# Performance work log

Hardware: AMD Instinct MI355X
Metric: run time of the kernel (lower is better)

The kernel has to match this reference:

```python
import jax, jax.numpy as jnp
import numpy as np

N_NODES = 50000
N_EDGES = 800000
D_IN = 128
D_H = 128
D_OUT = 2
N_GRAPHS = 512
EPS = 1e-5


def _sage(x, src, dst, Wl, bl, Wr):
    # mean aggregation of source features at destination nodes
    msum = jax.ops.segment_sum(x[src], dst, num_segments=N_NODES)
    deg = jax.ops.segment_sum(jnp.ones((src.shape[0],), x.dtype), dst, num_segments=N_NODES)
    agg = msum / jnp.clip(deg, 1.0)[:, None]
    return agg @ Wl.T + bl + x @ Wr.T


def _bn(x, g, b, m, v):
    return (x - m) * jax.lax.rsqrt(v + EPS) * g + b


def setup_inputs() -> dict:
    key = jax.random.key(0)
    ks = jax.random.split(key, 24)
    s = lambda k, shape, fan: (jax.random.normal(k, shape, jnp.float32) / np.sqrt(fan))
    x = jax.random.normal(ks[0], (N_NODES, D_IN), jnp.float32)
    edge_index = jax.random.randint(ks[1], (2, N_EDGES), 0, N_NODES, jnp.int64)
    batch = jnp.sort(jax.random.randint(ks[2], (N_NODES,), 0, N_GRAPHS, jnp.int64))
    inp = {"x": x, "edge_index": edge_index, "batch": batch}
    # SAGEConv layers: lin_l (with bias) on aggregated, lin_r (no bias) on root
    dims = [(D_IN, D_H), (D_H, D_H), (D_H, D_OUT)]
    for i, (di, do) in enumerate(dims):
        inp[f"Wl{i}"] = s(ks[3 + 3 * i], (do, di), di)
        inp[f"bl{i}"] = jnp.zeros((do,), jnp.float32)
        inp[f"Wr{i}"] = s(ks[4 + 3 * i], (do, di), di)
    # BatchNorm (eval mode: running stats)
    for i in range(2):
        inp[f"g{i}"] = jnp.ones((D_H,), jnp.float32)
        inp[f"b{i}"] = jnp.zeros((D_H,), jnp.float32)
        inp[f"m{i}"] = 0.1 * jax.random.normal(ks[12 + 2 * i], (D_H,), jnp.float32)
        inp[f"v{i}"] = jax.random.uniform(ks[13 + 2 * i], (D_H,), jnp.float32, 0.5, 1.5)
    # graph prediction MLP: Linear(2*D_OUT, D_H) -> ReLU -> Linear(D_H, D_OUT)
    inp["mW1"] = s(ks[20], (D_H, 2 * D_OUT), 2 * D_OUT)
    inp["mb1"] = jnp.zeros((D_H,), jnp.float32)
    inp["mW2"] = s(ks[21], (D_OUT, D_H), D_H)
    inp["mb2"] = jnp.zeros((D_OUT,), jnp.float32)
    return inp


def reference(x, edge_index, batch, Wl0, bl0, Wr0, Wl1, bl1, Wr1, Wl2, bl2, Wr2,
              g0, b0, m0, v0, g1, b1, m1, v1, mW1, mb1, mW2, mb2):
    src, dst = edge_index[0], edge_index[1]
    h = _sage(x, src, dst, Wl0, bl0, Wr0)
    h = jax.nn.relu(_bn(h, g0, b0, m0, v0))  # dropout inactive in eval
    h = _sage(h, src, dst, Wl1, bl1, Wr1)
    h = jax.nn.relu(_bn(h, g1, b1, m1, v1))
    h = _sage(h, src, dst, Wl2, bl2, Wr2)  # [N, D_OUT]
    # global mean + max pooling per graph
    cnt = jax.ops.segment_sum(jnp.ones((h.shape[0],), h.dtype), batch, num_segments=N_GRAPHS)
    pmean = jax.ops.segment_sum(h, batch, num_segments=N_GRAPHS) / jnp.clip(cnt, 1.0)[:, None]
    pmax = jax.ops.segment_max(h, batch, num_segments=N_GRAPHS)
    g = jnp.concatenate([pmean, pmax], axis=1)  # [G, 2*D_OUT]
    g = jax.nn.relu(g @ mW1.T + mb1)
    return g @ mW2.T + mb2  # [G, D_OUT]
```

## Files before the change

### kernel.cpp

```cpp
#include <hip/hip_runtime.h>
#include <hip/hip_bf16.h>
#include <float.h>

#define N_NODES 50000
#define N_EDGES 800000
#define D_H 128
#define N_GRAPHS 512
#define EPSV 1e-5f
#define NB_SCAN ((N_NODES + 255) / 256)

__device__ __forceinline__ void atomicMaxF(float* addr, float val) {
    if (val >= 0.0f) atomicMax((int*)addr, __float_as_int(val));
    else atomicMin((unsigned int*)addr, (unsigned int)__float_as_int(val));
}

__global__ void hist_kernel(const int* __restrict__ dst, int* __restrict__ cnt) {
    int e = blockIdx.x * blockDim.x + threadIdx.x;
    if (e < N_EDGES) atomicAdd(&cnt[dst[e]], 1);
}

__global__ __launch_bounds__(256) void scan_local_kernel(const int* __restrict__ cnt,
                                                         int* __restrict__ row_ptr,
                                                         int* __restrict__ bsum) {
    __shared__ int sh[256];
    int t = threadIdx.x;
    int i = blockIdx.x * 256 + t;
    int v = (i < N_NODES) ? cnt[i] : 0;
    sh[t] = v;
    __syncthreads();
    int x = v;
    for (int off = 1; off < 256; off <<= 1) {
        int y = (t >= off) ? sh[t - off] : 0;
        __syncthreads();
        x += y;
        sh[t] = x;
        __syncthreads();
    }
    if (i < N_NODES) row_ptr[i] = x - v;
    if (t == 255) bsum[blockIdx.x] = x;
}

__global__ __launch_bounds__(256) void scan_bsum_kernel(const int* __restrict__ bsum,
                                                        int* __restrict__ bofs) {
    __shared__ int sh[256];
    int t = threadIdx.x;
    int v = (t < NB_SCAN) ? bsum[t] : 0;
    sh[t] = v;
    __syncthreads();
    int x = v;
    for (int off = 1; off < 256; off <<= 1) {
        int y = (t >= off) ? sh[t - off] : 0;
        __syncthreads();
        x += y;
        sh[t] = x;
        __syncthreads();
    }
    if (t < NB_SCAN) bofs[t] = x - v;
}

__global__ __launch_bounds__(256) void scan_add_kernel(int* __restrict__ row_ptr,
                                                       int* __restrict__ wofs,
                                                       const int* __restrict__ bofs,
                                                       float* __restrict__ psum,
                                                       float* __restrict__ pcnt,
                                                       float* __restrict__ pmax) {
    int t = threadIdx.x;
    int i = blockIdx.x * 256 + t;
    if (i < N_NODES) {
        int r = row_ptr[i] + bofs[blockIdx.x];
        row_ptr[i] = r;
        wofs[i] = r;
    }
    if (i == 0) row_ptr[N_NODES] = N_EDGES;
    if (i < N_GRAPHS * 2) { psum[i] = 0.f; pmax[i] = -FLT_MAX; }
    if (i < N_GRAPHS) pcnt[i] = 0.f;
}

__global__ void scatter_kernel(const int* __restrict__ src, const int* __restrict__ dst,
                               int* __restrict__ wofs, int* __restrict__ csr_src) {
    int e = blockIdx.x * blockDim.x + threadIdx.x;
    if (e < N_EDGES) {
        int pos = atomicAdd(&wofs[dst[e]], 1);
        csr_src[pos] = src[e];
    }
}

#define ROWS 32
#define RPW 8
template <int MODE>
__global__ __launch_bounds__(256, 6) void fused_sage_kernel(
    const float* __restrict__ xin,
    const int* __restrict__ row_ptr, const int* __restrict__ csr_src,
    const float* __restrict__ Wl, const float* __restrict__ bl,
    const float* __restrict__ Wr,
    const float* __restrict__ gg, const float* __restrict__ bb,
    const float* __restrict__ mm, const float* __restrict__ vv,
    float* __restrict__ hout,
    const float* __restrict__ Wl2, const float* __restrict__ Wr2,
    float* __restrict__ p2r2) {
    __shared__ float s_agg[ROWS][D_H];
    __shared__ float s_x[ROWS][D_H];
    int row0 = blockIdx.x * ROWS;
    int t = threadIdx.x;
    int lane = t & 63;
    int w = t >> 6;

    const float2* xp = (const float2*)xin;

    for (int rr = 0; rr < RPW; rr++) {
        int r = w * RPW + rr;
        int row = row0 + r;
        float2 vx = make_float2(0.f, 0.f);
        float ax = 0.f, ay = 0.f;
        if (row < N_NODES) {
            vx = xp[(size_t)row * 64 + lane];
            int s0 = row_ptr[row], s1 = row_ptr[row + 1];
            int e = s0;
            for (; e + 7 < s1; e += 8) {
                int i0 = csr_src[e],     i1 = csr_src[e + 1];
                int i2 = csr_src[e + 2], i3 = csr_src[e + 3];
                int i4 = csr_src[e + 4], i5 = csr_src[e + 5];
                int i6 = csr_src[e + 6], i7 = csr_src[e + 7];
                float2 v0 = xp[(size_t)i0 * 64 + lane];
                float2 v1 = xp[(size_t)i1 * 64 + lane];
                float2 v2 = xp[(size_t)i2 * 64 + lane];
                float2 v3 = xp[(size_t)i3 * 64 + lane];
                float2 v4 = xp[(size_t)i4 * 64 + lane];
                float2 v5 = xp[(size_t)i5 * 64 + lane];
                float2 v6 = xp[(size_t)i6 * 64 + lane];
                float2 v7 = xp[(size_t)i7 * 64 + lane];
                ax += ((v0.x + v1.x) + (v2.x + v3.x)) + ((v4.x + v5.x) + (v6.x + v7.x));
                ay += ((v0.y + v1.y) + (v2.y + v3.y)) + ((v4.y + v5.y) + (v6.y + v7.y));
            }
            for (; e + 1 < s1; e += 2) {
                int i0 = csr_src[e], i1 = csr_src[e + 1];
                float2 v0 = xp[(size_t)i0 * 64 + lane];
                float2 v1 = xp[(size_t)i1 * 64 + lane];
                ax += v0.x + v1.x;
                ay += v0.y + v1.y;
            }
            if (e < s1) {
                float2 v0 = xp[(size_t)csr_src[e] * 64 + lane];
                ax += v0.x;
                ay += v0.y;
            }
            float inv = 1.0f / (float)max(s1 - s0, 1);
            ax *= inv;
            ay *= inv;
        }
        ((float2*)s_x[r])[lane] = vx;
        ((float2*)s_agg[r])[lane] = make_float2(ax, ay);
    }

    int j = lane;
    const float4* wl0 = (const float4*)(Wl + (size_t)j * D_H);
    const float4* wl1 = (const float4*)(Wl + (size_t)(j + 64) * D_H);
    const float4* wr0 = (const float4*)(Wr + (size_t)j * D_H);
    const float4* wr1 = (const float4*)(Wr + (size_t)(j + 64) * D_H);

    float acc0[RPW], acc1[RPW];
#pragma unroll
    for (int r = 0; r < RPW; r++) { acc0[r] = 0.f; acc1[r] = 0.f; }

    for (int k0 = 0; k0 < D_H / 4; k0 += 2) {
        float4 a0[2], a1[2], b0[2], b1[2];
#pragma unroll
        for (int q = 0; q < 2; q++) {
            a0[q] = wl0[k0 + q];
            a1[q] = wl1[k0 + q];
            b0[q] = wr0[k0 + q];
            b1[q] = wr1[k0 + q];
        }
#pragma unroll
        for (int r = 0; r < RPW; r++) {
            int row = w * RPW + r;
#pragma unroll
            for (int q = 0; q < 2; q++) {
                float4 xa = ((const float4*)s_agg[row])[k0 + q];
                float4 xx = ((const float4*)s_x[row])[k0 + q];
                acc0[r] += xa.x * a0[q].x + xa.y * a0[q].y + xa.z * a0[q].z + xa.w * a0[q].w
                         + xx.x * b0[q].x + xx.y * b0[q].y + xx.z * b0[q].z + xx.w * b0[q].w;
                acc1[r] += xa.x * a1[q].x + xa.y * a1[q].y + xa.z * a1[q].z + xa.w * a1[q].w
                         + xx.x * b1[q].x + xx.y * b1[q].y + xx.z * b1[q].z + xx.w * b1[q].w;
            }
        }
    }

    float sc0 = gg[j] * rsqrtf(vv[j] + EPSV);
    float sh0 = bb[j] + (bl[j] - mm[j]) * sc0;
    float sc1 = gg[j + 64] * rsqrtf(vv[j + 64] + EPSV);
    float sh1 = bb[j + 64] + (bl[j + 64] - mm[j + 64]) * sc1;

    if (MODE == 0) {
#pragma unroll
        for (int r = 0; r < RPW; r++) {
            int row = row0 + w * RPW + r;
            if (row < N_NODES) {
                hout[(size_t)row * D_H + j] = fmaxf(acc0[r] * sc0 + sh0, 0.f);
                hout[(size_t)row * D_H + j + 64] = fmaxf(acc1[r] * sc1 + sh1, 0.f);
            }
        }
    } else {
        float wl2_0a = Wl2[j],       wl2_0b = Wl2[j + 64];
        float wl2_1a = Wl2[128 + j], wl2_1b = Wl2[192 + j];
        float wr2_0a = Wr2[j],       wr2_0b = Wr2[j + 64];
        float wr2_1a = Wr2[128 + j], wr2_1b = Wr2[192 + j];
#pragma unroll
        for (int r = 0; r < RPW; r++) {
            float v0 = fmaxf(acc0[r] * sc0 + sh0, 0.f);
            float v1 = fmaxf(acc1[r] * sc1 + sh1, 0.f);
            float p0 = v0 * wl2_0a + v1 * wl2_0b;
            float p1 = v0 * wl2_1a + v1 * wl2_1b;
            float p2 = v0 * wr2_0a + v1 * wr2_0b;
            float p3 = v0 * wr2_1a + v1 * wr2_1b;
            for (int off = 32; off; off >>= 1) {
                p0 += __shfl_down(p0, off);
                p1 += __shfl_down(p1, off);
                p2 += __shfl_down(p2, off);
                p3 += __shfl_down(p3, off);
            }
            int row = row0 + w * RPW + r;
            if (lane == 0 && row < N_NODES)
                ((float4*)p2r2)[row] = make_float4(p0, p1, p2, p3);
        }
    }
}

__global__ __launch_bounds__(256) void aggpool_kernel(
    const float* __restrict__ p2r2, const int* __restrict__ row_ptr,
    const int* __restrict__ csr_src, const int* __restrict__ batch,
    const float* __restrict__ bl2,
    float* __restrict__ psum, float* __restrict__ pcnt, float* __restrict__ pmax) {
    int i = blockIdx.x * blockDim.x + threadIdx.x;
    if (i >= N_NODES) return;
    int s0 = row_ptr[i], s1 = row_ptr[i + 1];
    float a0 = 0.f, a1 = 0.f;
    int e = s0;
    for (; e + 3 < s1; e += 4) {
        float2 v0 = ((const float2*)p2r2)[(size_t)csr_src[e] * 2];
        float2 v1 = ((const float2*)p2r2)[(size_t)csr_src[e + 1] * 2];
        float2 v2 = ((const float2*)p2r2)[(size_t)csr_src[e + 2] * 2];
        float2 v3 = ((const float2*)p2r2)[(size_t)csr_src[e + 3] * 2];
        a0 += (v0.x + v1.x) + (v2.x + v3.x);
        a1 += (v0.y + v1.y) + (v2.y + v3.y);
    }
    for (; e < s1; e++) {
        float2 v = ((const float2*)p2r2)[(size_t)csr_src[e] * 2];
        a0 += v.x;
        a1 += v.y;
    }
    float inv = 1.0f / (float)max(s1 - s0, 1);
    float2 r = ((const float2*)p2r2)[(size_t)i * 2 + 1];
    float h0 = a0 * inv + bl2[0] + r.x;
    float h1 = a1 * inv + bl2[1] + r.y;
    int b = batch[i];
    atomicAdd(&psum[b * 2], h0);
    atomicAdd(&psum[b * 2 + 1], h1);
    atomicAdd(&pcnt[b], 1.0f);
    atomicMaxF(&pmax[b * 2], h0);
    atomicMaxF(&pmax[b * 2 + 1], h1);
}

__global__ __launch_bounds__(128) void mlp_kernel(
    const float* __restrict__ psum, const float* __restrict__ pcnt,
    const float* __restrict__ pmax,
    const float* __restrict__ mW1, const float* __restrict__ mb1,
    const float* __restrict__ mW2, const float* __restrict__ mb2,
    float* __restrict__ out) {
    int b = blockIdx.x;
    int t = threadIdx.x;
    float cntv = fmaxf(pcnt[b], 1.0f);
    float g0 = psum[b * 2] / cntv;
    float g1 = psum[b * 2 + 1] / cntv;
    float g2 = pmax[b * 2];
    float g3 = pmax[b * 2 + 1];
    float4 w = ((const float4*)mW1)[t];
    float h = fmaxf(g0 * w.x + g1 * w.y + g2 * w.z + g3 * w.w + mb1[t], 0.f);
    float o0 = h * mW2[t];
    float o1 = h * mW2[128 + t];
    for (int off = 32; off; off >>= 1) {
        o0 += __shfl_down(o0, off);
        o1 += __shfl_down(o1, off);
    }
    __shared__ float sh[4];
    if ((t & 63) == 0) {
        sh[(t >> 6) * 2] = o0;
        sh[(t >> 6) * 2 + 1] = o1;
    }
    __syncthreads();
    if (t == 0) {
        out[b * 2] = sh[0] + sh[2] + mb2[0];
        out[b * 2 + 1] = sh[1] + sh[3] + mb2[1];
    }
}

extern "C" void kernel_launch(void* const* d_in, const int* in_sizes, int n_in,
                              void* d_out, int out_size, void* d_ws, size_t ws_size,
                              hipStream_t stream) {
    const float* x = (const float*)d_in[0];
    const int* ei = (const int*)d_in[1];
    const int* batch = (const int*)d_in[2];
    const float* Wl0 = (const float*)d_in[3];
    const float* bl0 = (const float*)d_in[4];
    const float* Wr0 = (const float*)d_in[5];
    const float* Wl1 = (const float*)d_in[6];
    const float* bl1 = (const float*)d_in[7];
    const float* Wr1 = (const float*)d_in[8];
    const float* Wl2 = (const float*)d_in[9];
    const float* bl2 = (const float*)d_in[10];
    const float* Wr2 = (const float*)d_in[11];
    const float* g0 = (const float*)d_in[12];
    const float* b0 = (const float*)d_in[13];
    const float* m0 = (const float*)d_in[14];
    const float* v0 = (const float*)d_in[15];
    const float* g1 = (const float*)d_in[16];
    const float* b1 = (const float*)d_in[17];
    const float* m1 = (const float*)d_in[18];
    const float* v1 = (const float*)d_in[19];
    const float* mW1 = (const float*)d_in[20];
    const float* mb1 = (const float*)d_in[21];
    const float* mW2 = (const float*)d_in[22];
    const float* mb2 = (const float*)d_in[23];

    const int* src = ei;
    const int* dst = ei + N_EDGES;

    char* ws = (char*)d_ws;
    size_t off = 0;
    auto alloc = [&](size_t bytes) -> char* {
        char* p = ws + off;
        off += (bytes + 255) & ~(size_t)255;
        return p;
    };
    int* cnt = (int*)alloc((size_t)N_NODES * 4);
    int* row_ptr = (int*)alloc((size_t)(N_NODES + 1) * 4);
    int* wofs = (int*)alloc((size_t)N_NODES * 4);
    int* csr_src = (int*)alloc((size_t)N_EDGES * 4);
    float* h0 = (float*)alloc((size_t)N_NODES * D_H * 4);
    float* p2r2 = (float*)alloc((size_t)N_NODES * 16);
    float* psum = (float*)alloc((size_t)N_GRAPHS * 2 * 4);
    float* pcnt = (float*)alloc((size_t)N_GRAPHS * 4);
    float* pmax = (float*)alloc((size_t)N_GRAPHS * 2 * 4);
    int* bsum = (int*)alloc((size_t)NB_SCAN * 4);
    int* bofs = (int*)alloc((size_t)NB_SCAN * 4);
    (void)ws_size;

    hipMemsetAsync(cnt, 0, (size_t)N_NODES * 4, stream);
    hist_kernel<<<(N_EDGES + 255) / 256, 256, 0, stream>>>(dst, cnt);
    scan_local_kernel<<<NB_SCAN, 256, 0, stream>>>(cnt, row_ptr, bsum);
    scan_bsum_kernel<<<1, 256, 0, stream>>>(bsum, bofs);
    scan_add_kernel<<<NB_SCAN, 256, 0, stream>>>(row_ptr, wofs, bofs, psum, pcnt, pmax);
    scatter_kernel<<<(N_EDGES + 255) / 256, 256, 0, stream>>>(src, dst, wofs, csr_src);

    int nblk = (N_NODES + ROWS - 1) / ROWS;

    fused_sage_kernel<0><<<nblk, 256, 0, stream>>>(
        x, row_ptr, csr_src, Wl0, bl0, Wr0, g0, b0, m0, v0, h0,
        nullptr, nullptr, nullptr);

    fused_sage_kernel<1><<<nblk, 256, 0, stream>>>(
        h0, row_ptr, csr_src, Wl1, bl1, Wr1, g1, b1, m1, v1, nullptr,
        Wl2, Wr2, p2r2);

    aggpool_kernel<<<(N_NODES + 255) / 256, 256, 0, stream>>>(
        p2r2, row_ptr, csr_src, batch, bl2, psum, pcnt, pmax);

    mlp_kernel<<<N_GRAPHS, 128, 0, stream>>>(psum, pcnt, pmax, mW1, mb1, mW2, mb2,
                                             (float*)d_out);
}
```

Baseline: 608.2 us.

## Stream edges per warp with double-buffered prefetch and fold block-offset scan

```diff
diff --git a/kernel.cpp b/kernel.cpp
--- a/kernel.cpp
+++ b/kernel.cpp
@@ -40,34 +40,25 @@
     if (t == 255) bsum[blockIdx.x] = x;
 }
 
-__global__ __launch_bounds__(256) void scan_bsum_kernel(const int* __restrict__ bsum,
-                                                        int* __restrict__ bofs) {
-    __shared__ int sh[256];
-    int t = threadIdx.x;
-    int v = (t < NB_SCAN) ? bsum[t] : 0;
-    sh[t] = v;
-    __syncthreads();
-    int x = v;
-    for (int off = 1; off < 256; off <<= 1) {
-        int y = (t >= off) ? sh[t - off] : 0;
-        __syncthreads();
-        x += y;
-        sh[t] = x;
-        __syncthreads();
-    }
-    if (t < NB_SCAN) bofs[t] = x - v;
-}
-
 __global__ __launch_bounds__(256) void scan_add_kernel(int* __restrict__ row_ptr,
                                                        int* __restrict__ wofs,
-                                                       const int* __restrict__ bofs,
+                                                       const int* __restrict__ bsum,
                                                        float* __restrict__ psum,
                                                        float* __restrict__ pcnt,
                                                        float* __restrict__ pmax) {
+    __shared__ int sh[256];
     int t = threadIdx.x;
+    int v = (t < NB_SCAN && t < blockIdx.x) ? bsum[t] : 0;
+    sh[t] = v;
+    __syncthreads();
+    for (int off = 128; off; off >>= 1) {
+        if (t < off) sh[t] += sh[t + off];
+        __syncthreads();
+    }
+    int bofs = sh[0];
     int i = blockIdx.x * 256 + t;
     if (i < N_NODES) {
-        int r = row_ptr[i] + bofs[blockIdx.x];
+        int r = row_ptr[i] + bofs;
         row_ptr[i] = r;
         wofs[i] = r;
     }
@@ -88,7 +79,7 @@
 #define ROWS 32
 #define RPW 8
 template <int MODE>
-__global__ __launch_bounds__(256, 6) void fused_sage_kernel(
+__global__ __launch_bounds__(256, 4) void fused_sage_kernel(
     const float* __restrict__ xin,
     const int* __restrict__ row_ptr, const int* __restrict__ csr_src,
     const float* __restrict__ Wl, const float* __restrict__ bl,
@@ -107,49 +98,79 @@
 
     const float2* xp = (const float2*)xin;
 
+#pragma unroll
     for (int rr = 0; rr < RPW; rr++) {
         int r = w * RPW + rr;
         int row = row0 + r;
         float2 vx = make_float2(0.f, 0.f);
+        if (row < N_NODES) vx = xp[(size_t)row * 64 + lane];
+        ((float2*)s_x[r])[lane] = vx;
+    }
+
+    int rbeg = row0 + w * RPW;
+    int rwend = rbeg + RPW; if (rwend > N_NODES) rwend = N_NODES;
+    if (rbeg < N_NODES) {
+        int E0 = row_ptr[rbeg];
+        int E1 = row_ptr[rwend];
+        int cur = rbeg;
+        int cur_start = E0;
+        int cur_end = row_ptr[cur + 1];
         float ax = 0.f, ay = 0.f;
-        if (row < N_NODES) {
-            vx = xp[(size_t)row * 64 + lane];
-            int s0 = row_ptr[row], s1 = row_ptr[row + 1];
-            int e = s0;
-            for (; e + 7 < s1; e += 8) {
-                int i0 = csr_src[e],     i1 = csr_src[e + 1];
-                int i2 = csr_src[e + 2], i3 = csr_src[e + 3];
-                int i4 = csr_src[e + 4], i5 = csr_src[e + 5];
-                int i6 = csr_src[e + 6], i7 = csr_src[e + 7];
-                float2 v0 = xp[(size_t)i0 * 64 + lane];
-                float2 v1 = xp[(size_t)i1 * 64 + lane];
-                float2 v2 = xp[(size_t)i2 * 64 + lane];
-                float2 v3 = xp[(size_t)i3 * 64 + lane];
-                float2 v4 = xp[(size_t)i4 * 64 + lane];
-                float2 v5 = xp[(size_t)i5 * 64 + lane];
-                float2 v6 = xp[(size_t)i6 * 64 + lane];
-                float2 v7 = xp[(size_t)i7 * 64 + lane];
-                ax += ((v0.x + v1.x) + (v2.x + v3.x)) + ((v4.x + v5.x) + (v6.x + v7.x));
-                ay += ((v0.y + v1.y) + (v2.y + v3.y)) + ((v4.y + v5.y) + (v6.y + v7.y));
-            }
-            for (; e + 1 < s1; e += 2) {
-                int i0 = csr_src[e], i1 = csr_src[e + 1];
-                float2 v0 = xp[(size_t)i0 * 64 + lane];
-                float2 v1 = xp[(size_t)i1 * 64 + lane];
-                ax += v0.x + v1.x;
-                ay += v0.y + v1.y;
-            }
-            if (e < s1) {
-                float2 v0 = xp[(size_t)csr_src[e] * 64 + lane];
-                ax += v0.x;
-                ay += v0.y;
-            }
-            float inv = 1.0f / (float)max(s1 - s0, 1);
-            ax *= inv;
-            ay *= inv;
-        }
-        ((float2*)s_x[r])[lane] = vx;
-        ((float2*)s_agg[r])[lane] = make_float2(ax, ay);
+
+        int iA[8]; float2 vA[8];
+        int iB[8]; float2 vB[8];
+
+        auto prefetch = [&](int* I, float2* V, int cbase) {
+#pragma unroll
+            for (int k = 0; k < 8; k++) {
+                int e = cbase + k;
+                I[k] = csr_src[(e < E1) ? e : (E1 - 1)];
+            }
+#pragma unroll
+            for (int k = 0; k < 8; k++) V[k] = xp[(size_t)I[k] * 64 + lane];
+        };
+        auto consume = [&](const float2* V, int cbase) {
+#pragma unroll
+            for (int k = 0; k < 8; k++) {
+                int epos = cbase + k;
+                if (epos < E1) {
+                    while (epos >= cur_end) {
+                        float inv = 1.0f / (float)max(cur_end - cur_start, 1);
+                        ((float2*)s_agg[cur - row0])[lane] =
+                            make_float2(ax * inv, ay * inv);
+                        ax = 0.f; ay = 0.f;
+                        cur++;
+                        cur_start = cur_end;
+                        cur_end = row_ptr[cur + 1];
+                    }
+                    ax += V[k].x;
+                    ay += V[k].y;
+                }
+            }
+        };
+
+        int base = E0;
+        bool useA = true;
+        if (base < E1) prefetch(iA, vA, base);
+        while (base < E1) {
+            int nb = base + 8;
+            if (useA) {
+                if (nb < E1) prefetch(iB, vB, nb);
+                consume(vA, base);
+            } else {
+                if (nb < E1) prefetch(iA, vA, nb);
+                consume(vB, base);
+            }
+            useA = !useA;
+            base = nb;
+        }
+        while (cur < rwend) {
+            float inv = 1.0f / (float)max(cur_end - cur_start, 1);
+            ((float2*)s_agg[cur - row0])[lane] = make_float2(ax * inv, ay * inv);
+            ax = 0.f; ay = 0.f;
+            cur++;
+            if (cur < rwend) { cur_start = cur_end; cur_end = row_ptr[cur + 1]; }
+        }
     }
 
     int j = lane;
@@ -342,14 +363,12 @@
     float* pcnt = (float*)alloc((size_t)N_GRAPHS * 4);
     float* pmax = (float*)alloc((size_t)N_GRAPHS * 2 * 4);
     int* bsum = (int*)alloc((size_t)NB_SCAN * 4);
-    int* bofs = (int*)alloc((size_t)NB_SCAN * 4);
     (void)ws_size;
 
     hipMemsetAsync(cnt, 0, (size_t)N_NODES * 4, stream);
     hist_kernel<<<(N_EDGES + 255) / 256, 256, 0, stream>>>(dst, cnt);
     scan_local_kernel<<<NB_SCAN, 256, 0, stream>>>(cnt, row_ptr, bsum);
-    scan_bsum_kernel<<<1, 256, 0, stream>>>(bsum, bofs);
-    scan_add_kernel<<<NB_SCAN, 256, 0, stream>>>(row_ptr, wofs, bofs, psum, pcnt, pmax);
+    scan_add_kernel<<<NB_SCAN, 256, 0, stream>>>(row_ptr, wofs, bsum, psum, pcnt, pmax);
     scatter_kernel<<<(N_EDGES + 255) / 256, 256, 0, stream>>>(src, dst, wofs, csr_src);
 
     int nblk = (N_NODES + ROWS - 1) / ROWS;
```

After: 596.7 us. Within noise of the previous version (-1.9%).
